# Kernel tuning notes

Measured on AMD Instinct MI355X. Metric: run time of the kernel, lower is better.

The kernel has to match this reference:

```python
import jax, jax.numpy as jnp
import numpy as np

BATCH_SIZE = 8
INPUT_AXIS = 3
A = BATCH_SIZE * INPUT_AXIS          # 24
D = BATCH_SIZE * (INPUT_AXIS - 1)    # 16

# encoder layer dims (out, in), decoder layer dims (out, in)
_ENC = [(A, A), (A, A), (A, A), (D, A)]
_DEC = [(A, D), (A, A), (A, A), (A, A)]


def setup_inputs() -> dict:
    key = jax.random.key(0)
    ks = jax.random.split(key, 1 + 2 * (len(_ENC) + len(_DEC)))
    inp = {"x": jax.random.normal(ks[0], (A,), dtype=jnp.float32)}
    i = 1
    for j, (o, n) in enumerate(_ENC):
        inp[f"enc_w{j}"] = jax.random.normal(ks[i], (o, n), dtype=jnp.float32) * (1.0 / np.sqrt(n)); i += 1
        inp[f"enc_b{j}"] = jax.random.normal(ks[i], (o,), dtype=jnp.float32) * 0.01; i += 1
    for j, (o, n) in enumerate(_DEC):
        inp[f"dec_w{j}"] = jax.random.normal(ks[i], (o, n), dtype=jnp.float32) * (1.0 / np.sqrt(n)); i += 1
        inp[f"dec_b{j}"] = jax.random.normal(ks[i], (o,), dtype=jnp.float32) * 0.01; i += 1
    return inp


def _forward(x, enc_w0, enc_b0, enc_w1, enc_b1, enc_w2, enc_b2, enc_w3, enc_b3,
             dec_w0, dec_b0, dec_w1, dec_b1, dec_w2, dec_b2, dec_w3, dec_b3):
    h = jax.nn.relu(enc_w0 @ x + enc_b0)
    h = jax.nn.relu(enc_w1 @ h + enc_b1)
    h = jax.nn.relu(enc_w2 @ h + enc_b2)
    y = enc_w3 @ h + enc_b3

    in_data = x.reshape(BATCH_SIZE, INPUT_AXIS)          # [8,3]
    lat_repr = y.reshape(BATCH_SIZE, INPUT_AXIS - 1)     # [8,2]

    # pairwise L2 distances over rows of in_data (the in_min offset cancels in the subtraction,
    # exactly as in the torch code: (in_min+a)-(in_min+b) == a-b)
    diffs = in_data[:, None, :] - in_data[None, :, :]    # [8,8,3]
    in_diff_sum = jnp.sqrt(jnp.sum(diffs * diffs, axis=-1)).reshape(-1)  # [64]

    # FAITHFUL BUG REPRODUCTION: the original's second loop reuses the stale
    # in_cord1/in_cord2 from the last iteration of the first loop (n=m=7),
    # so every entry is sqrt(sum((in_data[7]-in_data[7])**2)) == 0.
    z = in_data[BATCH_SIZE - 1] - in_data[BATCH_SIZE - 1]
    lat_diff_sum = jnp.repeat(jnp.sqrt(jnp.sum(z * z)), BATCH_SIZE * BATCH_SIZE)  # [64]

    d = jax.nn.relu(dec_w0 @ y + dec_b0)
    d = jax.nn.relu(dec_w1 @ d + dec_b1)
    d = jax.nn.relu(dec_w2 @ d + dec_b2)
    out = jnp.tanh(dec_w3 @ d + dec_b3)
    return out, in_diff_sum, lat_diff_sum, lat_repr


def reference(x, enc_w0, enc_b0, enc_w1, enc_b1, enc_w2, enc_b2, enc_w3, enc_b3,
              dec_w0, dec_b0, dec_w1, dec_b1, dec_w2, dec_b2, dec_w3, dec_b3):
    return _forward(x, enc_w0, enc_b0, enc_w1, enc_b1, enc_w2, enc_b2, enc_w3, enc_b3,
                    dec_w0, dec_b0, dec_w1, dec_b1, dec_w2, dec_b2, dec_w3, dec_b3)
```

## Files before the change

kernel.cpp:

```cpp
#include <hip/hip_runtime.h>
#include <math.h>


#define AE_A 24
#define AE_D 16

__global__ __launch_bounds__(64) void ae_fwd_kernel(
    const float* __restrict__ x,
    const float* __restrict__ ew0, const float* __restrict__ eb0,
    const float* __restrict__ ew1, const float* __restrict__ eb1,
    const float* __restrict__ ew2, const float* __restrict__ eb2,
    const float* __restrict__ ew3, const float* __restrict__ eb3,
    const float* __restrict__ dw0, const float* __restrict__ db0,
    const float* __restrict__ dw1, const float* __restrict__ db1,
    const float* __restrict__ dw2, const float* __restrict__ db2,
    const float* __restrict__ dw3, const float* __restrict__ db3,
    float* __restrict__ out)
{
    __shared__ float xs[AE_A];
    __shared__ float ha[AE_A];
    __shared__ float hb[AE_A];
    __shared__ float y[AE_D];

    const int t = threadIdx.x;

    if (t < AE_A) xs[t] = x[t];
    __syncthreads();

    {
        const int m = t >> 3;
        const int n = t & 7;
        const float d0 = xs[m * 3 + 0] - xs[n * 3 + 0];
        const float d1 = xs[m * 3 + 1] - xs[n * 3 + 1];
        const float d2 = xs[m * 3 + 2] - xs[n * 3 + 2];
        out[24 + t] = sqrtf(d0 * d0 + d1 * d1 + d2 * d2);
        out[88 + t] = 0.0f;
    }

    if (t < AE_A) {
        float acc = eb0[t];
        #pragma unroll
        for (int k = 0; k < AE_A; ++k) acc += ew0[t * AE_A + k] * xs[k];
        ha[t] = fmaxf(acc, 0.0f);
    }
    __syncthreads();

    if (t < AE_A) {
        float acc = eb1[t];
        #pragma unroll
        for (int k = 0; k < AE_A; ++k) acc += ew1[t * AE_A + k] * ha[k];
        hb[t] = fmaxf(acc, 0.0f);
    }
    __syncthreads();

    if (t < AE_A) {
        float acc = eb2[t];
        #pragma unroll
        for (int k = 0; k < AE_A; ++k) acc += ew2[t * AE_A + k] * hb[k];
        ha[t] = fmaxf(acc, 0.0f);
    }
    __syncthreads();

    if (t < AE_D) {
        float acc = eb3[t];
        #pragma unroll
        for (int k = 0; k < AE_A; ++k) acc += ew3[t * AE_A + k] * ha[k];
        y[t] = acc;
        out[152 + t] = acc;
    }
    __syncthreads();

    if (t < AE_A) {
        float acc = db0[t];
        #pragma unroll
        for (int k = 0; k < AE_D; ++k) acc += dw0[t * AE_D + k] * y[k];
        ha[t] = fmaxf(acc, 0.0f);
    }
    __syncthreads();

    if (t < AE_A) {
        float acc = db1[t];
        #pragma unroll
        for (int k = 0; k < AE_A; ++k) acc += dw1[t * AE_A + k] * ha[k];
        hb[t] = fmaxf(acc, 0.0f);
    }
    __syncthreads();

    if (t < AE_A) {
        float acc = db2[t];
        #pragma unroll
        for (int k = 0; k < AE_A; ++k) acc += dw2[t * AE_A + k] * hb[k];
        ha[t] = fmaxf(acc, 0.0f);
    }
    __syncthreads();

    if (t < AE_A) {
        float acc = db3[t];
        #pragma unroll
        for (int k = 0; k < AE_A; ++k) acc += dw3[t * AE_A + k] * ha[k];
        out[t] = tanhf(acc);
    }
}

extern "C" void kernel_launch(void* const* d_in, const int* in_sizes, int n_in,
                              void* d_out, int out_size, void* d_ws, size_t ws_size,
                              hipStream_t stream) {
    (void)in_sizes; (void)n_in; (void)d_ws; (void)ws_size; (void)out_size;

    const float* x   = (const float*)d_in[0];
    const float* ew0 = (const float*)d_in[1];
    const float* eb0 = (const float*)d_in[2];
    const float* ew1 = (const float*)d_in[3];
    const float* eb1 = (const float*)d_in[4];
    const float* ew2 = (const float*)d_in[5];
    const float* eb2 = (const float*)d_in[6];
    const float* ew3 = (const float*)d_in[7];
    const float* eb3 = (const float*)d_in[8];
    const float* dw0 = (const float*)d_in[9];
    const float* db0 = (const float*)d_in[10];
    const float* dw1 = (const float*)d_in[11];
    const float* db1 = (const float*)d_in[12];
    const float* dw2 = (const float*)d_in[13];
    const float* db2 = (const float*)d_in[14];
    const float* dw3 = (const float*)d_in[15];
    const float* db3 = (const float*)d_in[16];
    float* out = (float*)d_out;

    ae_fwd_kernel<<<1, 64, 0, stream>>>(
        x, ew0, eb0, ew1, eb1, ew2, eb2, ew3, eb3,
        dw0, db0, dw1, db1, dw2, db2, dw3, db3, out);
}
```

Before: 9.557 us.

## Prefetch all weights into padded LDS up front with 256 threads

```diff
diff --git a/kernel.cpp b/kernel.cpp
--- a/kernel.cpp
+++ b/kernel.cpp
@@ -4,8 +4,56 @@
 
 #define AE_A 24
 #define AE_D 16
+#define NT   256
 
-__global__ __launch_bounds__(64) void ae_fwd_kernel(
+constexpr int OF_EW0 = 0;
+constexpr int OF_EW1 = OF_EW0 + 600;
+constexpr int OF_EW2 = OF_EW1 + 600;
+constexpr int OF_EW3 = OF_EW2 + 600;
+constexpr int OF_DW0 = OF_EW3 + 400;
+constexpr int OF_DW1 = OF_DW0 + 408;
+constexpr int OF_DW2 = OF_DW1 + 600;
+constexpr int OF_DW3 = OF_DW2 + 600;
+constexpr int OF_EB0 = OF_DW3 + 600;
+constexpr int OF_EB1 = OF_EB0 + 24;
+constexpr int OF_EB2 = OF_EB1 + 24;
+constexpr int OF_EB3 = OF_EB2 + 24;
+constexpr int OF_DB0 = OF_EB3 + 16;
+constexpr int OF_DB1 = OF_DB0 + 24;
+constexpr int OF_DB2 = OF_DB1 + 24;
+constexpr int OF_DB3 = OF_DB2 + 24;
+constexpr int OF_X   = OF_DB3 + 24;
+constexpr int OF_HA  = OF_X + 24;
+constexpr int OF_HB  = OF_HA + 24;
+constexpr int OF_Y   = OF_HB + 24;
+constexpr int LDS_TOT = OF_Y + 16;
+
+template <int ROWS, int COLS, int STRIDE>
+__device__ __forceinline__ void stage(float* __restrict__ dst,
+                                      const float* __restrict__ src, int tid) {
+    constexpr int N = ROWS * COLS;
+    #pragma unroll
+    for (int base = 0; base < N; base += NT) {
+        const int i = base + tid;
+        if (i < N) dst[(i / COLS) * STRIDE + (i % COLS)] = src[i];
+    }
+}
+
+template <int K>
+__device__ __forceinline__ float dotk(const float* __restrict__ w,
+                                      const float* __restrict__ h, float bias) {
+    float a0 = bias, a1 = 0.f, a2 = 0.f, a3 = 0.f;
+    #pragma unroll
+    for (int k = 0; k < K; k += 4) {
+        a0 = fmaf(w[k + 0], h[k + 0], a0);
+        a1 = fmaf(w[k + 1], h[k + 1], a1);
+        a2 = fmaf(w[k + 2], h[k + 2], a2);
+        a3 = fmaf(w[k + 3], h[k + 3], a3);
+    }
+    return (a0 + a1) + (a2 + a3);
+}
+
+__global__ __launch_bounds__(NT) void ae_fwd_kernel(
     const float* __restrict__ x,
     const float* __restrict__ ew0, const float* __restrict__ eb0,
     const float* __restrict__ ew1, const float* __restrict__ eb1,
@@ -17,89 +65,67 @@
     const float* __restrict__ dw3, const float* __restrict__ db3,
     float* __restrict__ out)
 {
-    __shared__ float xs[AE_A];
-    __shared__ float ha[AE_A];
-    __shared__ float hb[AE_A];
-    __shared__ float y[AE_D];
-
+    __shared__ float L[LDS_TOT];
     const int t = threadIdx.x;
 
-    if (t < AE_A) xs[t] = x[t];
+    stage<AE_A, AE_A, 25>(&L[OF_EW0], ew0, t);
+    stage<AE_A, AE_A, 25>(&L[OF_EW1], ew1, t);
+    stage<AE_A, AE_A, 25>(&L[OF_EW2], ew2, t);
+    stage<AE_D, AE_A, 25>(&L[OF_EW3], ew3, t);
+    stage<AE_A, AE_D, 17>(&L[OF_DW0], dw0, t);
+    stage<AE_A, AE_A, 25>(&L[OF_DW1], dw1, t);
+    stage<AE_A, AE_A, 25>(&L[OF_DW2], dw2, t);
+    stage<AE_A, AE_A, 25>(&L[OF_DW3], dw3, t);
+    if (t < AE_A) {
+        L[OF_EB0 + t] = eb0[t];
+        L[OF_EB1 + t] = eb1[t];
+        L[OF_EB2 + t] = eb2[t];
+        L[OF_DB0 + t] = db0[t];
+        L[OF_DB1 + t] = db1[t];
+        L[OF_DB2 + t] = db2[t];
+        L[OF_DB3 + t] = db3[t];
+        L[OF_X   + t] = x[t];
+    }
+    if (t < AE_D) L[OF_EB3 + t] = eb3[t];
     __syncthreads();
 
-    {
-        const int m = t >> 3;
-        const int n = t & 7;
-        const float d0 = xs[m * 3 + 0] - xs[n * 3 + 0];
-        const float d1 = xs[m * 3 + 1] - xs[n * 3 + 1];
-        const float d2 = xs[m * 3 + 2] - xs[n * 3 + 2];
-        out[24 + t] = sqrtf(d0 * d0 + d1 * d1 + d2 * d2);
-        out[88 + t] = 0.0f;
+    if (t >= 64 && t < 128) {
+        const int p = t - 64;
+        const int m = p >> 3;
+        const int n = p & 7;
+        const float d0 = L[OF_X + m * 3 + 0] - L[OF_X + n * 3 + 0];
+        const float d1 = L[OF_X + m * 3 + 1] - L[OF_X + n * 3 + 1];
+        const float d2 = L[OF_X + m * 3 + 2] - L[OF_X + n * 3 + 2];
+        out[24 + p] = sqrtf(d0 * d0 + d1 * d1 + d2 * d2);
+        out[88 + p] = 0.0f;
     }
 
-    if (t < AE_A) {
-        float acc = eb0[t];
-        #pragma unroll
-        for (int k = 0; k < AE_A; ++k) acc += ew0[t * AE_A + k] * xs[k];
-        ha[t] = fmaxf(acc, 0.0f);
-    }
+    if (t < AE_A)
+        L[OF_HA + t] = fmaxf(dotk<AE_A>(&L[OF_EW0 + t * 25], &L[OF_X], L[OF_EB0 + t]), 0.f);
     __syncthreads();
-
-    if (t < AE_A) {
-        float acc = eb1[t];
-        #pragma unroll
-        for (int k = 0; k < AE_A; ++k) acc += ew1[t * AE_A + k] * ha[k];
-        hb[t] = fmaxf(acc, 0.0f);
-    }
+    if (t < AE_A)
+        L[OF_HB + t] = fmaxf(dotk<AE_A>(&L[OF_EW1 + t * 25], &L[OF_HA], L[OF_EB1 + t]), 0.f);
     __syncthreads();
-
-    if (t < AE_A) {
-        float acc = eb2[t];
-        #pragma unroll
-        for (int k = 0; k < AE_A; ++k) acc += ew2[t * AE_A + k] * hb[k];
-        ha[t] = fmaxf(acc, 0.0f);
-    }
+    if (t < AE_A)
+        L[OF_HA + t] = fmaxf(dotk<AE_A>(&L[OF_EW2 + t * 25], &L[OF_HB], L[OF_EB2 + t]), 0.f);
     __syncthreads();
-
     if (t < AE_D) {
-        float acc = eb3[t];
-        #pragma unroll
-        for (int k = 0; k < AE_A; ++k) acc += ew3[t * AE_A + k] * ha[k];
-        y[t] = acc;
+        const float acc = dotk<AE_A>(&L[OF_EW3 + t * 25], &L[OF_HA], L[OF_EB3 + t]);
+        L[OF_Y + t] = acc;
         out[152 + t] = acc;
     }
     __syncthreads();
-
-    if (t < AE_A) {
-        float acc = db0[t];
-        #pragma unroll
-        for (int k = 0; k < AE_D; ++k) acc += dw0[t * AE_D + k] * y[k];
-        ha[t] = fmaxf(acc, 0.0f);
-    }
+    if (t < AE_A)
+        L[OF_HA + t] = fmaxf(dotk<AE_D>(&L[OF_DW0 + t * 17], &L[OF_Y], L[OF_DB0 + t]), 0.f);
     __syncthreads();
-
-    if (t < AE_A) {
-        float acc = db1[t];
-        #pragma unroll
-        for (int k = 0; k < AE_A; ++k) acc += dw1[t * AE_A + k] * ha[k];
-        hb[t] = fmaxf(acc, 0.0f);
-    }
+    if (t < AE_A)
+        L[OF_HB + t] = fmaxf(dotk<AE_A>(&L[OF_DW1 + t * 25], &L[OF_HA], L[OF_DB1 + t]), 0.f);
     __syncthreads();
-
-    if (t < AE_A) {
-        float acc = db2[t];
-        #pragma unroll
-        for (int k = 0; k < AE_A; ++k) acc += dw2[t * AE_A + k] * hb[k];
-        ha[t] = fmaxf(acc, 0.0f);
-    }
+    if (t < AE_A)
+        L[OF_HA + t] = fmaxf(dotk<AE_A>(&L[OF_DW2 + t * 25], &L[OF_HB], L[OF_DB2 + t]), 0.f);
     __syncthreads();
-
-    if (t < AE_A) {
-        float acc = db3[t];
-        #pragma unroll
-        for (int k = 0; k < AE_A; ++k) acc += dw3[t * AE_A + k] * ha[k];
-        out[t] = tanhf(acc);
-    }
+    if (t < AE_A)
+        out[t] = tanhf(dotk<AE_A>(&L[OF_DW3 + t * 25], &L[OF_HA], L[OF_DB3 + t]));
 }
 
 extern "C" void kernel_launch(void* const* d_in, const int* in_sizes, int n_in,
@@ -126,7 +152,7 @@
     const float* db3 = (const float*)d_in[16];
     float* out = (float*)d_out;
 
-    ae_fwd_kernel<<<1, 64, 0, stream>>>(
+    ae_fwd_kernel<<<1, NT, 0, stream>>>(
         x, ew0, eb0, ew1, eb1, ew2, eb2, ew3, eb3,
         dw0, db0, dw1, db1, dw2, db2, dw3, db3, out);
 }
```

Result: slower. 10.77 us (+12.7%).

## Use register-resident weights with wave shuffles and prefetch next layer's weights

Applied to the files above, without the earlier changes.

```diff
diff --git a/kernel.cpp b/kernel.cpp
--- a/kernel.cpp
+++ b/kernel.cpp
@@ -4,6 +4,37 @@
 
 #define AE_A 24
 #define AE_D 16
+
+__device__ __forceinline__ void ld24(float* __restrict__ w, const float* __restrict__ p) {
+    const float4* q = (const float4*)p;
+    #pragma unroll
+    for (int i = 0; i < 6; ++i) {
+        float4 v = q[i];
+        w[4 * i + 0] = v.x; w[4 * i + 1] = v.y; w[4 * i + 2] = v.z; w[4 * i + 3] = v.w;
+    }
+}
+
+__device__ __forceinline__ void ld16(float* __restrict__ w, const float* __restrict__ p) {
+    const float4* q = (const float4*)p;
+    #pragma unroll
+    for (int i = 0; i < 4; ++i) {
+        float4 v = q[i];
+        w[4 * i + 0] = v.x; w[4 * i + 1] = v.y; w[4 * i + 2] = v.z; w[4 * i + 3] = v.w;
+    }
+}
+
+template <int K>
+__device__ __forceinline__ float dot_shfl(const float* __restrict__ w, float h, float bias) {
+    float a0 = bias, a1 = 0.f, a2 = 0.f, a3 = 0.f;
+    #pragma unroll
+    for (int k = 0; k < K; k += 4) {
+        a0 = fmaf(w[k + 0], __shfl(h, k + 0), a0);
+        a1 = fmaf(w[k + 1], __shfl(h, k + 1), a1);
+        a2 = fmaf(w[k + 2], __shfl(h, k + 2), a2);
+        a3 = fmaf(w[k + 3], __shfl(h, k + 3), a3);
+    }
+    return (a0 + a1) + (a2 + a3);
+}
 
 __global__ __launch_bounds__(64) void ae_fwd_kernel(
     const float* __restrict__ x,
@@ -17,89 +48,51 @@
     const float* __restrict__ dw3, const float* __restrict__ db3,
     float* __restrict__ out)
 {
-    __shared__ float xs[AE_A];
-    __shared__ float ha[AE_A];
-    __shared__ float hb[AE_A];
-    __shared__ float y[AE_D];
+    const int t   = threadIdx.x;
+    const int r24 = t < AE_A ? t : AE_A - 1;
+    const int r16 = t < AE_D ? t : AE_D - 1;
 
-    const int t = threadIdx.x;
+    float wa[AE_A], wb[AE_A];
 
-    if (t < AE_A) xs[t] = x[t];
-    __syncthreads();
+    ld24(wa, ew0 + r24 * AE_A);
+    const float xv = x[r24];
+    const float b0 = eb0[r24], b1 = eb1[r24], b2 = eb2[r24];
+    const float b3 = eb3[r16];
+    const float b4 = db0[r24], b5 = db1[r24], b6 = db2[r24], b7 = db3[r24];
 
     {
-        const int m = t >> 3;
-        const int n = t & 7;
-        const float d0 = xs[m * 3 + 0] - xs[n * 3 + 0];
-        const float d1 = xs[m * 3 + 1] - xs[n * 3 + 1];
-        const float d2 = xs[m * 3 + 2] - xs[n * 3 + 2];
+        const int m = t >> 3, n = t & 7;
+        const float d0 = __shfl(xv, m * 3 + 0) - __shfl(xv, n * 3 + 0);
+        const float d1 = __shfl(xv, m * 3 + 1) - __shfl(xv, n * 3 + 1);
+        const float d2 = __shfl(xv, m * 3 + 2) - __shfl(xv, n * 3 + 2);
         out[24 + t] = sqrtf(d0 * d0 + d1 * d1 + d2 * d2);
         out[88 + t] = 0.0f;
     }
 
-    if (t < AE_A) {
-        float acc = eb0[t];
-        #pragma unroll
-        for (int k = 0; k < AE_A; ++k) acc += ew0[t * AE_A + k] * xs[k];
-        ha[t] = fmaxf(acc, 0.0f);
-    }
-    __syncthreads();
+    ld24(wb, ew1 + r24 * AE_A);
+    float h = fmaxf(dot_shfl<AE_A>(wa, xv, b0), 0.f);
 
-    if (t < AE_A) {
-        float acc = eb1[t];
-        #pragma unroll
-        for (int k = 0; k < AE_A; ++k) acc += ew1[t * AE_A + k] * ha[k];
-        hb[t] = fmaxf(acc, 0.0f);
-    }
-    __syncthreads();
+    ld24(wa, ew2 + r24 * AE_A);
+    h = fmaxf(dot_shfl<AE_A>(wb, h, b1), 0.f);
 
-    if (t < AE_A) {
-        float acc = eb2[t];
-        #pragma unroll
-        for (int k = 0; k < AE_A; ++k) acc += ew2[t * AE_A + k] * hb[k];
-        ha[t] = fmaxf(acc, 0.0f);
-    }
-    __syncthreads();
+    ld24(wb, ew3 + r16 * AE_A);
+    h = fmaxf(dot_shfl<AE_A>(wa, h, b2), 0.f);
 
-    if (t < AE_D) {
-        float acc = eb3[t];
-        #pragma unroll
-        for (int k = 0; k < AE_A; ++k) acc += ew3[t * AE_A + k] * ha[k];
-        y[t] = acc;
-        out[152 + t] = acc;
-    }
-    __syncthreads();
+    ld16(wa, dw0 + r24 * AE_D);
+    const float y = dot_shfl<AE_A>(wb, h, b3);
+    if (t < AE_D) out[152 + t] = y;
 
-    if (t < AE_A) {
-        float acc = db0[t];
-        #pragma unroll
-        for (int k = 0; k < AE_D; ++k) acc += dw0[t * AE_D + k] * y[k];
-        ha[t] = fmaxf(acc, 0.0f);
-    }
-    __syncthreads();
+    ld24(wb, dw1 + r24 * AE_A);
+    h = fmaxf(dot_shfl<AE_D>(wa, y, b4), 0.f);
 
-    if (t < AE_A) {
-        float acc = db1[t];
-        #pragma unroll
-        for (int k = 0; k < AE_A; ++k) acc += dw1[t * AE_A + k] * ha[k];
-        hb[t] = fmaxf(acc, 0.0f);
-    }
-    __syncthreads();
+    ld24(wa, dw2 + r24 * AE_A);
+    h = fmaxf(dot_shfl<AE_A>(wb, h, b5), 0.f);
 
-    if (t < AE_A) {
-        float acc = db2[t];
-        #pragma unroll
-        for (int k = 0; k < AE_A; ++k) acc += dw2[t * AE_A + k] * hb[k];
-        ha[t] = fmaxf(acc, 0.0f);
-    }
-    __syncthreads();
+    ld24(wb, dw3 + r24 * AE_A);
+    h = fmaxf(dot_shfl<AE_A>(wa, h, b6), 0.f);
 
-    if (t < AE_A) {
-        float acc = db3[t];
-        #pragma unroll
-        for (int k = 0; k < AE_A; ++k) acc += dw3[t * AE_A + k] * ha[k];
-        out[t] = tanhf(acc);
-    }
+    h = tanhf(dot_shfl<AE_A>(wb, h, b7));
+    if (t < AE_A) out[t] = h;
 }
 
 extern "C" void kernel_launch(void* const* d_in, const int* in_sizes, int n_in,
```

Measured after the change: 9.680 us. About the same (+1.3%).
